# Kernel optimization log

Hardware: AMD Instinct MI355X
Metric: run time of the kernel (lower is better)

The kernel has to match this reference:

```python
import jax, jax.numpy as jnp
import numpy as np

B, Q, K, H = 4, 256, 256, 512
NEG = -1e9


def setup_inputs() -> dict:
    key = jax.random.key(0)
    ks = jax.random.split(key, 7)
    scale = 1.0 / np.sqrt(H)
    return {
        "query": jax.random.normal(ks[0], (B, Q, H), jnp.float32),
        "key": jax.random.normal(ks[1], (B, K, H), jnp.float32),
        "value": jax.random.normal(ks[2], (B, K, H), jnp.float32),
        "valid_lens": jax.random.randint(ks[3], (B,), 0, K, jnp.int32),
        "Wq": jax.random.normal(ks[4], (H, H), jnp.float32) * scale,
        "Wk": jax.random.normal(ks[5], (H, H), jnp.float32) * scale,
        "wv": jax.random.normal(ks[6], (H,), jnp.float32) * scale,
    }


def reference(query, key, value, valid_lens, Wq, Wk, wv):
    # projections (nn.Linear without bias)
    q = query @ Wq              # [B,Q,H]
    k = key @ Wk                # [B,K,H]
    # broadcast add + tanh: [B,Q,K,H]
    features = jnp.tanh(q[:, :, None, :] + k[:, None, :, :])
    # score projection w_v: [B,Q,K]
    scores = jnp.einsum("bqkh,h->bqk", features, wv)
    # sequence mask: positions >= valid_len masked out
    mask = jnp.arange(K)[None, :] >= valid_lens[:, None]   # [B,K]
    scores = jnp.where(mask[:, None, :], NEG, scores)
    attn = jax.nn.softmax(scores, axis=-1)                 # [B,Q,K]
    context = jnp.einsum("bqk,bkh->bqh", attn, value)      # [B,Q,H]
    return context
```

## Files before the change

kernel.cpp:

```cpp
#include <hip/hip_runtime.h>
#include <hip/hip_bf16.h>

#define B_ 4
#define Q_ 256
#define K_ 256
#define H_ 512
#define NEG (-1e9f)
#define PRESCALE 2.885390081777927f

typedef _Float16 half8 __attribute__((ext_vector_type(8)));
typedef float    f32x4 __attribute__((ext_vector_type(4)));

__global__ __launch_bounds__(512) void proj_kernel(
    const float* __restrict__ Xq, const float* __restrict__ Xk,
    const float* __restrict__ Wq, const float* __restrict__ Wk,
    float* __restrict__ Eq, float* __restrict__ EkT,
    const int* __restrict__ vlen)
{
    const int bx   = blockIdx.x;
    const int z    = bx >> 4;
    const int row0 = (bx & 15) * 64;
    const int bb   = row0 >> 8;
    const int k0   = row0 & 255;
    if (z && k0 >= vlen[bb]) return;

    const float* X = z ? Xk : Xq;
    const float* W = z ? Wk : Wq;

    __shared__ _Float16 Xl[2][8 * 520];
    __shared__ _Float16 Wl[2][8 * 520];

    const int col0 = blockIdx.y * 64;
    const int t    = threadIdx.x;
    const int lane = t & 63;
    const int wave = t >> 6;
    const int mw   = wave >> 1;
    const int nw   = wave & 1;
    const int m    = lane & 15;
    const int kgl  = lane >> 4;

    const int xr = t >> 3;
    const int xg = t & 7;
    const int wc = t & 63;
    const int wg = t >> 6;

    f32x4 acc[2] = {};

    float4 xv0 = *(const float4*)&X[(size_t)(row0 + xr) * H_ + xg * 8];
    float4 xv1 = *(const float4*)&X[(size_t)(row0 + xr) * H_ + xg * 8 + 4];
    float wv8[8];
    #pragma unroll
    for (int i = 0; i < 8; ++i)
        wv8[i] = W[(size_t)(wg * 8 + i) * H_ + col0 + wc];

    for (int it = 0; it < 8; ++it) {
        const int buf = it & 1;
        {
            half8 hx;
            hx[0] = (_Float16)xv0.x; hx[1] = (_Float16)xv0.y;
            hx[2] = (_Float16)xv0.z; hx[3] = (_Float16)xv0.w;
            hx[4] = (_Float16)xv1.x; hx[5] = (_Float16)xv1.y;
            hx[6] = (_Float16)xv1.z; hx[7] = (_Float16)xv1.w;
            *(half8*)&Xl[buf][xg * 520 + xr * 8] = hx;
            half8 hw;
            #pragma unroll
            for (int i = 0; i < 8; ++i) hw[i] = (_Float16)wv8[i];
            *(half8*)&Wl[buf][wg * 520 + wc * 8] = hw;
        }
        __syncthreads();
        if (it < 7) {
            const int kk = (it + 1) * 64;
            xv0 = *(const float4*)&X[(size_t)(row0 + xr) * H_ + kk + xg * 8];
            xv1 = *(const float4*)&X[(size_t)(row0 + xr) * H_ + kk + xg * 8 + 4];
            #pragma unroll
            for (int i = 0; i < 8; ++i)
                wv8[i] = W[(size_t)(kk + wg * 8 + i) * H_ + col0 + wc];
        }
        const _Float16* Asrc = z ? &Wl[buf][0] : &Xl[buf][0];
        const _Float16* Bsrc = z ? &Xl[buf][0] : &Wl[buf][0];
        #pragma unroll
        for (int ks = 0; ks < 2; ++ks) {
            const int slab = (ks * 4 + kgl) * 520;
            const half8 af = *(const half8*)&Asrc[slab + (16 * mw + m) * 8];
            #pragma unroll
            for (int nt = 0; nt < 2; ++nt) {
                const half8 bf =
                    *(const half8*)&Bsrc[slab + (nw * 32 + nt * 16 + m) * 8];
                acc[nt] = __builtin_amdgcn_mfma_f32_16x16x32_f16(af, bf, acc[nt], 0, 0, 0);
            }
        }
    }

    const int rloc = 16 * mw + kgl * 4;
    if (!z) {
        #pragma unroll
        for (int nt = 0; nt < 2; ++nt) {
            const int gcol = col0 + nw * 32 + nt * 16 + m;
            #pragma unroll
            for (int r = 0; r < 4; ++r)
                Eq[(size_t)(row0 + rloc + r) * H_ + gcol] =
                    __builtin_amdgcn_exp2f(acc[nt][r] * PRESCALE);
        }
    } else {
        #pragma unroll
        for (int nt = 0; nt < 2; ++nt) {
            const int gk = k0 + nw * 32 + nt * 16 + m;
            #pragma unroll
            for (int r = 0; r < 4; ++r)
                EkT[((size_t)bb * H_ + col0 + rloc + r) * K_ + gk] =
                    __builtin_amdgcn_exp2f(acc[nt][r] * PRESCALE);
        }
    }
}

__global__ __launch_bounds__(512) void fused_attn(
    const float* __restrict__ Eq, const float* __restrict__ EkT,
    const float* __restrict__ value, const int* __restrict__ vlen,
    const float* __restrict__ wv, float* __restrict__ out)
{
    const int qt = blockIdx.x;
    const int b  = blockIdx.y;
    const int q0 = qt * 4;
    const int t    = threadIdx.x;
    const int wave = t >> 6;
    const int lane = t & 63;

    __shared__ float eqh2[8 * 260];
    __shared__ float wm2[8 * 68];
    __shared__ float sc[4][K_];
    __shared__ float ctxp[4][4][H_];

    const int valid = vlen[b];

    {
        const int qi = t >> 7, p4 = (t & 127) * 4;
        const float4 v = *(const float4*)&Eq[((size_t)b * Q_ + q0 + qi) * H_ + p4];
        const float vv[4] = {v.x, v.y, v.z, v.w};
        const int sbase = (p4 >> 3) * 4;
        #pragma unroll
        for (int j = 0; j < 4; ++j)
            eqh2[((p4 & 7) + j) * 260 + sbase + qi] = vv[j];
        if (t < 128) {
            const float4 w = *(const float4*)&wv[t * 4];
            const float ww[4] = {w.x, w.y, w.z, w.w};
            #pragma unroll
            for (int j = 0; j < 4; ++j) {
                const int h = t * 4 + j;
                wm2[(h & 7) * 68 + (h >> 3)] = -2.f * ww[j];
            }
        }
    }
    __syncthreads();

    const int band = wave * 32;
    const int ho   = lane >> 3;
    const int kg   = lane & 7;
    const int kq   = band + kg * 4;

    if (band < valid) {
        const float* ekp = EkT + ((size_t)b * H_ + ho) * K_ + kq;
        float acc0[4] = {}, acc1[4] = {}, acc2[4] = {}, acc3[4] = {};
        float4 pe[4], n1[4], n2[4];
        #pragma unroll
        for (int p = 0; p < 4; ++p)
            pe[p] = *(const float4*)(ekp + (size_t)p * 8 * K_);
        #pragma unroll
        for (int p = 0; p < 4; ++p)
            n1[p] = *(const float4*)(ekp + (size_t)(4 + p) * 8 * K_);

        for (int g = 0; g < 16; ++g) {
            if (g < 14) {
                #pragma unroll
                for (int p = 0; p < 4; ++p)
                    n2[p] = *(const float4*)(ekp + (size_t)((g + 2) * 4 + p) * 8 * K_);
            }
            const float4 wv4 = *(const float4*)&wm2[ho * 68 + g * 4];
            const float wmp[4] = {wv4.x, wv4.y, wv4.z, wv4.w};
            #pragma unroll
            for (int p = 0; p < 4; ++p) {
                const float4 eq4 = *(const float4*)&eqh2[ho * 260 + (g * 4 + p) * 4];
                const float ek4[4] = {pe[p].x, pe[p].y, pe[p].z, pe[p].w};
                #pragma unroll
                for (int j = 0; j < 4; ++j) {
                    const float g0 = __builtin_fmaf(eq4.x, ek4[j], 1.0f);
                    acc0[j] = __builtin_fmaf(wmp[p], __builtin_amdgcn_rcpf(g0), acc0[j]);
                    const float g1 = __builtin_fmaf(eq4.y, ek4[j], 1.0f);
                    acc1[j] = __builtin_fmaf(wmp[p], __builtin_amdgcn_rcpf(g1), acc1[j]);
                    const float g2 = __builtin_fmaf(eq4.z, ek4[j], 1.0f);
                    acc2[j] = __builtin_fmaf(wmp[p], __builtin_amdgcn_rcpf(g2), acc2[j]);
                    const float g3 = __builtin_fmaf(eq4.w, ek4[j], 1.0f);
                    acc3[j] = __builtin_fmaf(wmp[p], __builtin_amdgcn_rcpf(g3), acc3[j]);
                }
            }
            #pragma unroll
            for (int p = 0; p < 4; ++p) { pe[p] = n1[p]; n1[p] = n2[p]; }
        }
        #pragma unroll
        for (int d = 8; d < 64; d <<= 1) {
            #pragma unroll
            for (int j = 0; j < 4; ++j) {
                acc0[j] += __shfl_xor(acc0[j], d);
                acc1[j] += __shfl_xor(acc1[j], d);
                acc2[j] += __shfl_xor(acc2[j], d);
                acc3[j] += __shfl_xor(acc3[j], d);
            }
        }
        if (ho == 0) {
            *(float4*)&sc[0][kq] = make_float4(acc0[0], acc0[1], acc0[2], acc0[3]);
            *(float4*)&sc[1][kq] = make_float4(acc1[0], acc1[1], acc1[2], acc1[3]);
            *(float4*)&sc[2][kq] = make_float4(acc2[0], acc2[1], acc2[2], acc2[3]);
            *(float4*)&sc[3][kq] = make_float4(acc3[0], acc3[1], acc3[2], acc3[3]);
        }
    }
    __syncthreads();

    if (wave < 4) {
        const int q = wave;
        if (valid == 0) {
            #pragma unroll
            for (int j = 0; j < 4; ++j) sc[q][lane + 64 * j] = 1.0f / K_;
        } else {
            float sv[4], mx = -3e38f;
            #pragma unroll
            for (int j = 0; j < 4; ++j) {
                const int kk = lane + 64 * j;
                const float s = (kk < valid) ? sc[q][kk] : NEG;
                sv[j] = s;
                mx = fmaxf(mx, s);
            }
            #pragma unroll
            for (int d = 32; d; d >>= 1) mx = fmaxf(mx, __shfl_xor(mx, d));
            float ev[4], sum = 0.f;
            #pragma unroll
            for (int j = 0; j < 4; ++j) { ev[j] = __expf(sv[j] - mx); sum += ev[j]; }
            #pragma unroll
            for (int d = 32; d; d >>= 1) sum += __shfl_xor(sum, d);
            const float inv = 1.0f / sum;
            #pragma unroll
            for (int j = 0; j < 4; ++j) sc[q][lane + 64 * j] = ev[j] * inv;
        }
    }
    __syncthreads();

    const int klim = (valid == 0) ? K_ : valid;
    const int kb   = wave * 32;
    const int kend = min(32, klim - kb);
    const int h0   = lane * 8;

    float c[4][8] = {};
    for (int kc = 0; kc < kend; ++kc) {
        const int kk = kb + kc;
        const float4* vp = (const float4*)&value[((size_t)b * K_ + kk) * H_ + h0];
        const float4 v0 = vp[0], v1 = vp[1];
        const float vr[8] = {v0.x, v0.y, v0.z, v0.w, v1.x, v1.y, v1.z, v1.w};
        const float a0 = sc[0][kk], a1 = sc[1][kk], a2 = sc[2][kk], a3 = sc[3][kk];
        #pragma unroll
        for (int j = 0; j < 8; ++j) {
            c[0][j] = __builtin_fmaf(a0, vr[j], c[0][j]);
            c[1][j] = __builtin_fmaf(a1, vr[j], c[1][j]);
            c[2][j] = __builtin_fmaf(a2, vr[j], c[2][j]);
            c[3][j] = __builtin_fmaf(a3, vr[j], c[3][j]);
        }
    }

    #define PARK(s)                                                           \
        do {                                                                  \
            _Pragma("unroll")                                                 \
            for (int qi = 0; qi < 4; ++qi) {                                  \
                float* d = &ctxp[s][qi][h0];                                  \
                ((float4*)d)[0] = make_float4(c[qi][0], c[qi][1], c[qi][2], c[qi][3]); \
                ((float4*)d)[1] = make_float4(c[qi][4], c[qi][5], c[qi][6], c[qi][7]); \
            }                                                                 \
        } while (0)
    #define FOLD(s)                                                           \
        do {                                                                  \
            _Pragma("unroll")                                                 \
            for (int qi = 0; qi < 4; ++qi) {                                  \
                const float* d = &ctxp[s][qi][h0];                            \
                _Pragma("unroll")                                             \
                for (int j = 0; j < 8; ++j) c[qi][j] += d[j];                 \
            }                                                                 \
        } while (0)

    if (wave >= 4) PARK(wave - 4);
    __syncthreads();
    if (wave < 4) FOLD(wave);
    __syncthreads();
    if (wave == 2 || wave == 3) PARK(wave - 2);
    __syncthreads();
    if (wave < 2) FOLD(wave);
    __syncthreads();
    if (wave == 1) PARK(1);
    __syncthreads();
    if (wave == 0) {
        FOLD(1);
        #pragma unroll
        for (int qi = 0; qi < 4; ++qi) {
            float* o = &out[((size_t)b * Q_ + q0 + qi) * H_ + h0];
            ((float4*)o)[0] = make_float4(c[qi][0], c[qi][1], c[qi][2], c[qi][3]);
            ((float4*)o)[1] = make_float4(c[qi][4], c[qi][5], c[qi][6], c[qi][7]);
        }
    }
    #undef PARK
    #undef FOLD
}

extern "C" void kernel_launch(void* const* d_in, const int* in_sizes, int n_in,
                              void* d_out, int out_size, void* d_ws, size_t ws_size,
                              hipStream_t stream)
{
    const float* query = (const float*)d_in[0];
    const float* key   = (const float*)d_in[1];
    const float* value = (const float*)d_in[2];
    const int*   vlen  = (const int*)  d_in[3];
    const float* Wq    = (const float*)d_in[4];
    const float* Wk    = (const float*)d_in[5];
    const float* wv    = (const float*)d_in[6];
    float*       outp  = (float*)d_out;

    float* EqBuf  = (float*)d_ws;
    float* EkTBuf = EqBuf + (size_t)B_ * Q_ * H_;

    dim3 g1(32, 8);
    proj_kernel<<<g1, 512, 0, stream>>>(query, key, Wq, Wk, EqBuf, EkTBuf, vlen);

    dim3 g2(Q_ / 4, B_);
    fused_attn<<<g2, 512, 0, stream>>>(EqBuf, EkTBuf, value, vlen, wv, outp);
}
```

Before: 36.65 us.

## Halve projection output tile, deepen global prefetch, prefetch value rows in context loop

The projection kernel now computes 64x32 output tiles instead of 64x64, doubling the grid so more blocks run concurrently. Each wave issues one MFMA per k-step, and only half the threads load W. Global loads are prefetched two stages ahead through register double-buffering. The attention context loop also software-prefetches the next value row, which hides load latency at the cost of more registers and redundant re-reads of X across the doubled column blocks.

```diff
diff --git a/kernel.cpp b/kernel.cpp
--- a/kernel.cpp
+++ b/kernel.cpp
@@ -28,88 +28,91 @@
     const float* W = z ? Wk : Wq;
 
     __shared__ _Float16 Xl[2][8 * 520];
-    __shared__ _Float16 Wl[2][8 * 520];
-
-    const int col0 = blockIdx.y * 64;
+    __shared__ _Float16 Wl[2][8 * 264];
+
+    const int col0 = blockIdx.y * 32;
     const int t    = threadIdx.x;
     const int lane = t & 63;
     const int wave = t >> 6;
-    const int mw   = wave >> 1;
-    const int nw   = wave & 1;
     const int m    = lane & 15;
     const int kgl  = lane >> 4;
 
-    const int xr = t >> 3;
-    const int xg = t & 7;
-    const int wc = t & 63;
-    const int wg = t >> 6;
-
-    f32x4 acc[2] = {};
-
-    float4 xv0 = *(const float4*)&X[(size_t)(row0 + xr) * H_ + xg * 8];
-    float4 xv1 = *(const float4*)&X[(size_t)(row0 + xr) * H_ + xg * 8 + 4];
-    float wv8[8];
+    const int aStrip = z ? (wave & 1) : (wave >> 1);
+    const int bStrip = z ? (wave >> 1) : (wave & 1);
+
+    const int xr  = t >> 3;
+    const int xg  = t & 7;
+    const int wc  = t & 31;
+    const int wg  = (t >> 5) & 7;
+    const bool doW = (t < 256);
+
+    f32x4 acc = {};
+
+    float4 xa[2], xb[2];
+    float  wr[2][8];
     #pragma unroll
-    for (int i = 0; i < 8; ++i)
-        wv8[i] = W[(size_t)(wg * 8 + i) * H_ + col0 + wc];
+    for (int s = 0; s < 2; ++s) {
+        const int kk = s * 64;
+        xa[s] = *(const float4*)&X[(size_t)(row0 + xr) * H_ + kk + xg * 8];
+        xb[s] = *(const float4*)&X[(size_t)(row0 + xr) * H_ + kk + xg * 8 + 4];
+        if (doW) {
+            #pragma unroll
+            for (int i = 0; i < 8; ++i)
+                wr[s][i] = W[(size_t)(kk + wg * 8 + i) * H_ + col0 + wc];
+        }
+    }
 
     for (int it = 0; it < 8; ++it) {
-        const int buf = it & 1;
+        const int s = it & 1;
         {
             half8 hx;
-            hx[0] = (_Float16)xv0.x; hx[1] = (_Float16)xv0.y;
-            hx[2] = (_Float16)xv0.z; hx[3] = (_Float16)xv0.w;
-            hx[4] = (_Float16)xv1.x; hx[5] = (_Float16)xv1.y;
-            hx[6] = (_Float16)xv1.z; hx[7] = (_Float16)xv1.w;
-            *(half8*)&Xl[buf][xg * 520 + xr * 8] = hx;
-            half8 hw;
-            #pragma unroll
-            for (int i = 0; i < 8; ++i) hw[i] = (_Float16)wv8[i];
-            *(half8*)&Wl[buf][wg * 520 + wc * 8] = hw;
+            hx[0] = (_Float16)xa[s].x; hx[1] = (_Float16)xa[s].y;
+            hx[2] = (_Float16)xa[s].z; hx[3] = (_Float16)xa[s].w;
+            hx[4] = (_Float16)xb[s].x; hx[5] = (_Float16)xb[s].y;
+            hx[6] = (_Float16)xb[s].z; hx[7] = (_Float16)xb[s].w;
+            *(half8*)&Xl[s][xg * 520 + xr * 8] = hx;
+            if (doW) {
+                half8 hw;
+                #pragma unroll
+                for (int i = 0; i < 8; ++i) hw[i] = (_Float16)wr[s][i];
+                *(half8*)&Wl[s][wg * 264 + wc * 8] = hw;
+            }
         }
         __syncthreads();
-        if (it < 7) {
-            const int kk = (it + 1) * 64;
-            xv0 = *(const float4*)&X[(size_t)(row0 + xr) * H_ + kk + xg * 8];
-            xv1 = *(const float4*)&X[(size_t)(row0 + xr) * H_ + kk + xg * 8 + 4];
-            #pragma unroll
-            for (int i = 0; i < 8; ++i)
-                wv8[i] = W[(size_t)(kk + wg * 8 + i) * H_ + col0 + wc];
-        }
-        const _Float16* Asrc = z ? &Wl[buf][0] : &Xl[buf][0];
-        const _Float16* Bsrc = z ? &Xl[buf][0] : &Wl[buf][0];
+        if (it + 2 < 8) {
+            const int kk = (it + 2) * 64;
+            xa[s] = *(const float4*)&X[(size_t)(row0 + xr) * H_ + kk + xg * 8];
+            xb[s] = *(const float4*)&X[(size_t)(row0 + xr) * H_ + kk + xg * 8 + 4];
+            if (doW) {
+                #pragma unroll
+                for (int i = 0; i < 8; ++i)
+                    wr[s][i] = W[(size_t)(kk + wg * 8 + i) * H_ + col0 + wc];
+            }
+        }
         #pragma unroll
         for (int ks = 0; ks < 2; ++ks) {
-            const int slab = (ks * 4 + kgl) * 520;
-            const half8 af = *(const half8*)&Asrc[slab + (16 * mw + m) * 8];
-            #pragma unroll
-            for (int nt = 0; nt < 2; ++nt) {
-                const half8 bf =
-                    *(const half8*)&Bsrc[slab + (nw * 32 + nt * 16 + m) * 8];
-                acc[nt] = __builtin_amdgcn_mfma_f32_16x16x32_f16(af, bf, acc[nt], 0, 0, 0);
-            }
-        }
-    }
-
-    const int rloc = 16 * mw + kgl * 4;
+            const int slab = ks * 4 + kgl;
+            const half8 xf = *(const half8*)&Xl[s][slab * 520 + ((z ? bStrip : aStrip) * 16 + m) * 8];
+            const half8 wf = *(const half8*)&Wl[s][slab * 264 + ((z ? aStrip : bStrip) * 16 + m) * 8];
+            const half8 af = z ? wf : xf;
+            const half8 bf = z ? xf : wf;
+            acc = __builtin_amdgcn_mfma_f32_16x16x32_f16(af, bf, acc, 0, 0, 0);
+        }
+    }
+
+    const int rsub = kgl * 4;
     if (!z) {
-        #pragma unroll
-        for (int nt = 0; nt < 2; ++nt) {
-            const int gcol = col0 + nw * 32 + nt * 16 + m;
-            #pragma unroll
-            for (int r = 0; r < 4; ++r)
-                Eq[(size_t)(row0 + rloc + r) * H_ + gcol] =
-                    __builtin_amdgcn_exp2f(acc[nt][r] * PRESCALE);
-        }
+        const int gcol = col0 + bStrip * 16 + m;
+        #pragma unroll
+        for (int r = 0; r < 4; ++r)
+            Eq[(size_t)(row0 + aStrip * 16 + rsub + r) * H_ + gcol] =
+                __builtin_amdgcn_exp2f(acc[r] * PRESCALE);
     } else {
-        #pragma unroll
-        for (int nt = 0; nt < 2; ++nt) {
-            const int gk = k0 + nw * 32 + nt * 16 + m;
-            #pragma unroll
-            for (int r = 0; r < 4; ++r)
-                EkT[((size_t)bb * H_ + col0 + rloc + r) * K_ + gk] =
-                    __builtin_amdgcn_exp2f(acc[nt][r] * PRESCALE);
-        }
+        const int gk = k0 + bStrip * 16 + m;
+        #pragma unroll
+        for (int r = 0; r < 4; ++r)
+            EkT[((size_t)bb * H_ + col0 + aStrip * 16 + rsub + r) * K_ + gk] =
+                __builtin_amdgcn_exp2f(acc[r] * PRESCALE);
     }
 }
 
@@ -248,11 +251,19 @@
     const int h0   = lane * 8;
 
     float c[4][8] = {};
+    float4 cv0, cv1;
+    if (kend > 0) {
+        const float4* vp = (const float4*)&value[((size_t)b * K_ + kb) * H_ + h0];
+        cv0 = vp[0]; cv1 = vp[1];
+    }
     for (int kc = 0; kc < kend; ++kc) {
         const int kk = kb + kc;
-        const float4* vp = (const float4*)&value[((size_t)b * K_ + kk) * H_ + h0];
-        const float4 v0 = vp[0], v1 = vp[1];
-        const float vr[8] = {v0.x, v0.y, v0.z, v0.w, v1.x, v1.y, v1.z, v1.w};
+        float4 nv0, nv1;
+        if (kc + 1 < kend) {
+            const float4* vp = (const float4*)&value[((size_t)b * K_ + kk + 1) * H_ + h0];
+            nv0 = vp[0]; nv1 = vp[1];
+        }
+        const float vr[8] = {cv0.x, cv0.y, cv0.z, cv0.w, cv1.x, cv1.y, cv1.z, cv1.w};
         const float a0 = sc[0][kk], a1 = sc[1][kk], a2 = sc[2][kk], a3 = sc[3][kk];
         #pragma unroll
         for (int j = 0; j < 8; ++j) {
@@ -261,6 +272,7 @@
             c[2][j] = __builtin_fmaf(a2, vr[j], c[2][j]);
             c[3][j] = __builtin_fmaf(a3, vr[j], c[3][j]);
         }
+        cv0 = nv0; cv1 = nv1;
     }
 
     #define PARK(s)                                                           \
@@ -321,7 +333,7 @@
     float* EqBuf  = (float*)d_ws;
     float* EkTBuf = EqBuf + (size_t)B_ * Q_ * H_;
 
-    dim3 g1(32, 8);
+    dim3 g1(32, 16);
     proj_kernel<<<g1, 512, 0, stream>>>(query, key, Wq, Wk, EqBuf, EkTBuf, vlen);
 
     dim3 g2(Q_ / 4, B_);
```

New measurement: 43.15 us. +17.7%, slower.

## Split hidden dimension across two wave groups with 1024-thread blocks for score computation

Applied to the files above, without the earlier changes.

Doubles the attention block to 1024 threads. The score phase now splits the hidden dimension into two halves, each handled by 8 waves, and writes partial scores to two shared buffers that are summed before softmax. The context phase stays on 8 waves and adds a one-row software prefetch of value rows. This aims to halve the serial latency of the rcp-heavy score loop per block, at the cost of higher register pressure under 1024-thread launch bounds and half the threads idling during the context phase.

```diff
diff --git a/kernel.cpp b/kernel.cpp
--- a/kernel.cpp
+++ b/kernel.cpp
@@ -113,7 +113,7 @@
     }
 }
 
-__global__ __launch_bounds__(512) void fused_attn(
+__global__ __launch_bounds__(1024) void fused_attn(
     const float* __restrict__ Eq, const float* __restrict__ EkT,
     const float* __restrict__ value, const int* __restrict__ vlen,
     const float* __restrict__ wv, float* __restrict__ out)
@@ -127,12 +127,12 @@
 
     __shared__ float eqh2[8 * 260];
     __shared__ float wm2[8 * 68];
-    __shared__ float sc[4][K_];
+    __shared__ float sc2[2][4][K_];
     __shared__ float ctxp[4][4][H_];
 
     const int valid = vlen[b];
 
-    {
+    if (t < 512) {
         const int qi = t >> 7, p4 = (t & 127) * 4;
         const float4 v = *(const float4*)&Eq[((size_t)b * Q_ + q0 + qi) * H_ + p4];
         const float vv[4] = {v.x, v.y, v.z, v.w};
@@ -140,25 +140,27 @@
         #pragma unroll
         for (int j = 0; j < 4; ++j)
             eqh2[((p4 & 7) + j) * 260 + sbase + qi] = vv[j];
-        if (t < 128) {
-            const float4 w = *(const float4*)&wv[t * 4];
-            const float ww[4] = {w.x, w.y, w.z, w.w};
-            #pragma unroll
-            for (int j = 0; j < 4; ++j) {
-                const int h = t * 4 + j;
-                wm2[(h & 7) * 68 + (h >> 3)] = -2.f * ww[j];
-            }
-        }
-    }
-    __syncthreads();
-
-    const int band = wave * 32;
+    } else if (t < 640) {
+        const int i = (t - 512) * 4;
+        const float4 w = *(const float4*)&wv[i];
+        const float ww[4] = {w.x, w.y, w.z, w.w};
+        #pragma unroll
+        for (int j = 0; j < 4; ++j) {
+            const int h = i + j;
+            wm2[(h & 7) * 68 + (h >> 3)] = -2.f * ww[j];
+        }
+    }
+    __syncthreads();
+
+    const int hh   = wave >> 3;
+    const int band = (wave & 7) * 32;
     const int ho   = lane >> 3;
     const int kg   = lane & 7;
     const int kq   = band + kg * 4;
 
     if (band < valid) {
-        const float* ekp = EkT + ((size_t)b * H_ + ho) * K_ + kq;
+        const float* ekp = EkT + ((size_t)b * H_ + hh * 256 + ho) * K_ + kq;
+        const int sb = hh * 32;
         float acc0[4] = {}, acc1[4] = {}, acc2[4] = {}, acc3[4] = {};
         float4 pe[4], n1[4], n2[4];
         #pragma unroll
@@ -168,17 +170,17 @@
         for (int p = 0; p < 4; ++p)
             n1[p] = *(const float4*)(ekp + (size_t)(4 + p) * 8 * K_);
 
-        for (int g = 0; g < 16; ++g) {
-            if (g < 14) {
+        for (int g = 0; g < 8; ++g) {
+            if (g < 6) {
                 #pragma unroll
                 for (int p = 0; p < 4; ++p)
                     n2[p] = *(const float4*)(ekp + (size_t)((g + 2) * 4 + p) * 8 * K_);
             }
-            const float4 wv4 = *(const float4*)&wm2[ho * 68 + g * 4];
+            const float4 wv4 = *(const float4*)&wm2[ho * 68 + sb + g * 4];
             const float wmp[4] = {wv4.x, wv4.y, wv4.z, wv4.w};
             #pragma unroll
             for (int p = 0; p < 4; ++p) {
-                const float4 eq4 = *(const float4*)&eqh2[ho * 260 + (g * 4 + p) * 4];
+                const float4 eq4 = *(const float4*)&eqh2[ho * 260 + (sb + g * 4 + p) * 4];
                 const float ek4[4] = {pe[p].x, pe[p].y, pe[p].z, pe[p].w};
                 #pragma unroll
                 for (int j = 0; j < 4; ++j) {
@@ -206,10 +208,10 @@
             }
         }
         if (ho == 0) {
-            *(float4*)&sc[0][kq] = make_float4(acc0[0], acc0[1], acc0[2], acc0[3]);
-            *(float4*)&sc[1][kq] = make_float4(acc1[0], acc1[1], acc1[2], acc1[3]);
-            *(float4*)&sc[2][kq] = make_float4(acc2[0], acc2[1], acc2[2], acc2[3]);
-            *(float4*)&sc[3][kq] = make_float4(acc3[0], acc3[1], acc3[2], acc3[3]);
+            *(float4*)&sc2[hh][0][kq] = make_float4(acc0[0], acc0[1], acc0[2], acc0[3]);
+            *(float4*)&sc2[hh][1][kq] = make_float4(acc1[0], acc1[1], acc1[2], acc1[3]);
+            *(float4*)&sc2[hh][2][kq] = make_float4(acc2[0], acc2[1], acc2[2], acc2[3]);
+            *(float4*)&sc2[hh][3][kq] = make_float4(acc3[0], acc3[1], acc3[2], acc3[3]);
         }
     }
     __syncthreads();
@@ -218,13 +220,14 @@
         const int q = wave;
         if (valid == 0) {
             #pragma unroll
-            for (int j = 0; j < 4; ++j) sc[q][lane + 64 * j] = 1.0f / K_;
+            for (int j = 0; j < 4; ++j) sc2[0][q][lane + 64 * j] = 1.0f / K_;
         } else {
             float sv[4], mx = -3e38f;
             #pragma unroll
             for (int j = 0; j < 4; ++j) {
                 const int kk = lane + 64 * j;
-                const float s = (kk < valid) ? sc[q][kk] : NEG;
+                const float s = (kk < valid)
+                    ? sc2[0][q][kk] + sc2[1][q][kk] : NEG;
                 sv[j] = s;
                 mx = fmaxf(mx, s);
             }
@@ -237,29 +240,40 @@
             for (int d = 32; d; d >>= 1) sum += __shfl_xor(sum, d);
             const float inv = 1.0f / sum;
             #pragma unroll
-            for (int j = 0; j < 4; ++j) sc[q][lane + 64 * j] = ev[j] * inv;
+            for (int j = 0; j < 4; ++j) sc2[0][q][lane + 64 * j] = ev[j] * inv;
         }
     }
     __syncthreads();
 
     const int klim = (valid == 0) ? K_ : valid;
-    const int kb   = wave * 32;
-    const int kend = min(32, klim - kb);
     const int h0   = lane * 8;
-
     float c[4][8] = {};
-    for (int kc = 0; kc < kend; ++kc) {
-        const int kk = kb + kc;
-        const float4* vp = (const float4*)&value[((size_t)b * K_ + kk) * H_ + h0];
-        const float4 v0 = vp[0], v1 = vp[1];
-        const float vr[8] = {v0.x, v0.y, v0.z, v0.w, v1.x, v1.y, v1.z, v1.w};
-        const float a0 = sc[0][kk], a1 = sc[1][kk], a2 = sc[2][kk], a3 = sc[3][kk];
-        #pragma unroll
-        for (int j = 0; j < 8; ++j) {
-            c[0][j] = __builtin_fmaf(a0, vr[j], c[0][j]);
-            c[1][j] = __builtin_fmaf(a1, vr[j], c[1][j]);
-            c[2][j] = __builtin_fmaf(a2, vr[j], c[2][j]);
-            c[3][j] = __builtin_fmaf(a3, vr[j], c[3][j]);
+    if (wave < 8) {
+        const int kb   = wave * 32;
+        const int kend = min(32, klim - kb);
+        float4 cv0, cv1;
+        if (kend > 0) {
+            const float4* vp = (const float4*)&value[((size_t)b * K_ + kb) * H_ + h0];
+            cv0 = vp[0]; cv1 = vp[1];
+        }
+        for (int kc = 0; kc < kend; ++kc) {
+            const int kk = kb + kc;
+            float4 nv0, nv1;
+            if (kc + 1 < kend) {
+                const float4* vp = (const float4*)&value[((size_t)b * K_ + kk + 1) * H_ + h0];
+                nv0 = vp[0]; nv1 = vp[1];
+            }
+            const float vr[8] = {cv0.x, cv0.y, cv0.z, cv0.w, cv1.x, cv1.y, cv1.z, cv1.w};
+            const float a0 = sc2[0][0][kk], a1 = sc2[0][1][kk];
+            const float a2 = sc2[0][2][kk], a3 = sc2[0][3][kk];
+            #pragma unroll
+            for (int j = 0; j < 8; ++j) {
+                c[0][j] = __builtin_fmaf(a0, vr[j], c[0][j]);
+                c[1][j] = __builtin_fmaf(a1, vr[j], c[1][j]);
+                c[2][j] = __builtin_fmaf(a2, vr[j], c[2][j]);
+                c[3][j] = __builtin_fmaf(a3, vr[j], c[3][j]);
+            }
+            cv0 = nv0; cv1 = nv1;
         }
     }
 
@@ -282,7 +296,7 @@
             }                                                                 \
         } while (0)
 
-    if (wave >= 4) PARK(wave - 4);
+    if (wave >= 4 && wave < 8) PARK(wave - 4);
     __syncthreads();
     if (wave < 4) FOLD(wave);
     __syncthreads();
@@ -325,5 +339,5 @@
     proj_kernel<<<g1, 512, 0, stream>>>(query, key, Wq, Wk, EqBuf, EkTBuf, vlen);
 
     dim3 g2(Q_ / 4, B_);
-    fused_attn<<<g2, 512, 0, stream>>>(EqBuf, EkTBuf, value, vlen, wv, outp);
+    fused_attn<<<g2, 1024, 0, stream>>>(EqBuf, EkTBuf, value, vlen, wv, outp);
 }
```

Result: slower. 96.05 us (median of 2 runs) (+162.1%).

## Share one reciprocal across four tanh terms and prefetch value rows

Applied to the files above, without the earlier changes.

The score inner loop now batches four reciprocals into one rcp of the product of four denominators, then recovers each reciprocal with multiplies (Montgomery trick). This cuts transcendental rcp instructions by four times at the cost of extra multiplies. Separately, the context loop software-prefetches the next value row into registers to hide global load latency. The product of four terms risks overflow or underflow in fp32 for large inputs, which could hurt accuracy.

```diff
diff --git a/kernel.cpp b/kernel.cpp
--- a/kernel.cpp
+++ b/kernel.cpp
@@ -179,18 +179,26 @@
             #pragma unroll
             for (int p = 0; p < 4; ++p) {
                 const float4 eq4 = *(const float4*)&eqh2[ho * 260 + (g * 4 + p) * 4];
-                const float ek4[4] = {pe[p].x, pe[p].y, pe[p].z, pe[p].w};
-                #pragma unroll
-                for (int j = 0; j < 4; ++j) {
-                    const float g0 = __builtin_fmaf(eq4.x, ek4[j], 1.0f);
-                    acc0[j] = __builtin_fmaf(wmp[p], __builtin_amdgcn_rcpf(g0), acc0[j]);
-                    const float g1 = __builtin_fmaf(eq4.y, ek4[j], 1.0f);
-                    acc1[j] = __builtin_fmaf(wmp[p], __builtin_amdgcn_rcpf(g1), acc1[j]);
-                    const float g2 = __builtin_fmaf(eq4.z, ek4[j], 1.0f);
-                    acc2[j] = __builtin_fmaf(wmp[p], __builtin_amdgcn_rcpf(g2), acc2[j]);
-                    const float g3 = __builtin_fmaf(eq4.w, ek4[j], 1.0f);
-                    acc3[j] = __builtin_fmaf(wmp[p], __builtin_amdgcn_rcpf(g3), acc3[j]);
-                }
+                const float w = wmp[p];
+                #define QUAD(EQ, ACC)                                           \
+                    do {                                                        \
+                        const float u0 = __builtin_fmaf(EQ, pe[p].x, 1.0f);     \
+                        const float u1 = __builtin_fmaf(EQ, pe[p].y, 1.0f);     \
+                        const float u2 = __builtin_fmaf(EQ, pe[p].z, 1.0f);     \
+                        const float u3 = __builtin_fmaf(EQ, pe[p].w, 1.0f);     \
+                        const float p01 = u0 * u1, p23 = u2 * u3;               \
+                        const float r = __builtin_amdgcn_rcpf(p01 * p23);       \
+                        const float rA = r * p23, rB = r * p01;                 \
+                        ACC[0] = __builtin_fmaf(w, rA * u1, ACC[0]);            \
+                        ACC[1] = __builtin_fmaf(w, rA * u0, ACC[1]);            \
+                        ACC[2] = __builtin_fmaf(w, rB * u3, ACC[2]);            \
+                        ACC[3] = __builtin_fmaf(w, rB * u2, ACC[3]);            \
+                    } while (0)
+                QUAD(eq4.x, acc0);
+                QUAD(eq4.y, acc1);
+                QUAD(eq4.z, acc2);
+                QUAD(eq4.w, acc3);
+                #undef QUAD
             }
             #pragma unroll
             for (int p = 0; p < 4; ++p) { pe[p] = n1[p]; n1[p] = n2[p]; }
@@ -248,11 +256,19 @@
     const int h0   = lane * 8;
 
     float c[4][8] = {};
+    float4 cv0, cv1;
+    if (kend > 0) {
+        const float4* vp = (const float4*)&value[((size_t)b * K_ + kb) * H_ + h0];
+        cv0 = vp[0]; cv1 = vp[1];
+    }
     for (int kc = 0; kc < kend; ++kc) {
         const int kk = kb + kc;
-        const float4* vp = (const float4*)&value[((size_t)b * K_ + kk) * H_ + h0];
-        const float4 v0 = vp[0], v1 = vp[1];
-        const float vr[8] = {v0.x, v0.y, v0.z, v0.w, v1.x, v1.y, v1.z, v1.w};
+        float4 nv0, nv1;
+        if (kc + 1 < kend) {
+            const float4* vp = (const float4*)&value[((size_t)b * K_ + kk + 1) * H_ + h0];
+            nv0 = vp[0]; nv1 = vp[1];
+        }
+        const float vr[8] = {cv0.x, cv0.y, cv0.z, cv0.w, cv1.x, cv1.y, cv1.z, cv1.w};
         const float a0 = sc[0][kk], a1 = sc[1][kk], a2 = sc[2][kk], a3 = sc[3][kk];
         #pragma unroll
         for (int j = 0; j < 8; ++j) {
@@ -261,6 +277,7 @@
             c[2][j] = __builtin_fmaf(a2, vr[j], c[2][j]);
             c[3][j] = __builtin_fmaf(a3, vr[j], c[3][j]);
         }
+        cv0 = nv0; cv1 = nv1;
     }
 
     #define PARK(s)                                                           \
```

New measurement: 46.06 us, median of 5. 25.7% more time.
